# Performance work log

Hardware: AMD Instinct MI355X
Metric: run time of the kernel (lower is better)

The kernel has to match this reference:

```python
import jax, jax.numpy as jnp
import numpy as np

EMB = 1024
HEADS = 16
FFN = 4096
EPS = 1e-5


def _layernorm(x, g, b):
    mu = jnp.mean(x, axis=-1, keepdims=True)
    var = jnp.mean((x - mu) ** 2, axis=-1, keepdims=True)
    return (x - mu) * jax.lax.rsqrt(var + EPS) * g + b


def setup_inputs() -> dict:
    key = jax.random.key(0)
    ks = jax.random.split(key, 8)
    B, T = 2, 2048
    s_in = 1.0 / np.sqrt(EMB)
    s_ffn = 1.0 / np.sqrt(FFN)
    return {
        "x": jax.random.normal(ks[0], (B, T, EMB), jnp.float32),
        "positions": jnp.arange(B * T, dtype=jnp.int64 if jax.config.jax_enable_x64 else jnp.int32).reshape(B, T),
        "ln1_g": jnp.ones((EMB,), jnp.float32),
        "ln1_b": jnp.zeros((EMB,), jnp.float32),
        "ln2_g": jnp.ones((EMB,), jnp.float32),
        "ln2_b": jnp.zeros((EMB,), jnp.float32),
        "Wq": jax.random.normal(ks[1], (EMB, EMB), jnp.float32) * s_in,
        "bq": jnp.zeros((EMB,), jnp.float32),
        "Wk": jax.random.normal(ks[2], (EMB, EMB), jnp.float32) * s_in,
        "bk": jnp.zeros((EMB,), jnp.float32),
        "Wv": jax.random.normal(ks[3], (EMB, EMB), jnp.float32) * s_in,
        "bv": jnp.zeros((EMB,), jnp.float32),
        "Wo": jax.random.normal(ks[4], (EMB, EMB), jnp.float32) * s_in,
        "bo": jnp.zeros((EMB,), jnp.float32),
        "W1": jax.random.normal(ks[5], (EMB, FFN), jnp.float32) * s_in,
        "b1": jnp.zeros((FFN,), jnp.float32),
        "W2": jax.random.normal(ks[6], (FFN, EMB), jnp.float32) * s_ffn,
        "b2": jnp.zeros((EMB,), jnp.float32),
    }


def reference(x, positions, ln1_g, ln1_b, ln2_g, ln2_b,
              Wq, bq, Wk, bk, Wv, bv, Wo, bo, W1, b1, W2, b2):
    B, T, C = x.shape
    H, D = HEADS, C // HEADS
    # x = ln1(x); then residual branches add onto the normalized x (as in source)
    x = _layernorm(x, ln1_g, ln1_b)
    # --- self attention (rope=None, mask=None, dropout inactive) ---
    q = (x @ Wq + bq).reshape(B, T, H, D).transpose(0, 2, 1, 3)  # [B,H,T,D]
    k = (x @ Wk + bk).reshape(B, T, H, D).transpose(0, 2, 1, 3)
    v = (x @ Wv + bv).reshape(B, T, H, D).transpose(0, 2, 1, 3)
    scale = 1.0 / jnp.sqrt(jnp.asarray(D, x.dtype))
    attn = jnp.einsum("bhtd,bhsd->bhts", q, k) * scale  # [B,H,T,T]
    attn = jax.nn.softmax(attn, axis=-1)
    attn_out = jnp.einsum("bhts,bhsd->bhtd", attn, v)
    attn_out = attn_out.transpose(0, 2, 1, 3).reshape(B, T, C)
    attn_out = attn_out @ Wo + bo
    x = x + attn_out
    # --- FFN with exact (erf) GELU, matching torch nn.GELU default ---
    h = _layernorm(x, ln2_g, ln2_b)
    h = jax.nn.gelu(h @ W1 + b1, approximate=False)
    h = h @ W2 + b2
    return x + h
```

## Files before the change

### kernel.cpp

```cpp
#include <hip/hip_runtime.h>
#include <cstdint>
#include <cstddef>

typedef __bf16 bf16;
typedef __bf16 bf16x8 __attribute__((ext_vector_type(8)));
typedef __bf16 bf16x4 __attribute__((ext_vector_type(4)));
typedef float f32x4 __attribute__((ext_vector_type(4)));

#define TOKENS 4096
#define TSEQ   2048
#define NHEADS 16
#define HDIM   64
#define CDIM   1024

typedef __attribute__((address_space(3))) unsigned int lds_uint;
typedef __attribute__((address_space(1))) const unsigned int g_uint;
__device__ __forceinline__ void glds16(const bf16* g, bf16* l) {
  __builtin_amdgcn_global_load_lds((g_uint*)g, (lds_uint*)l, 16, 0, 0);
}

#define NBUF 17
struct DetectArgs { const void* p[NBUF]; int n[NBUF]; };

__global__ __launch_bounds__(256) void detect_kernel(DetectArgs a, int* __restrict__ flags) {
  __shared__ int s_nz, s_bl;
  if (threadIdx.x == 0) { s_nz = 0; s_bl = 0; }
  __syncthreads();
  int i = blockIdx.x;
  const unsigned int* w = (const unsigned int*)a.p[i];
  int nwords = a.n[i] / 2; if (nwords > 2048) nwords = 2048;
  int nz = 0, bl = 0;
  for (int j = threadIdx.x; j < nwords; j += 256) {
    unsigned int v = w[j];
    if (v != 0u) {
      nz++;
      unsigned int e = (v >> 7) & 0xFFu;
      if (e >= 100u && e <= 140u) bl++;
    }
  }
  atomicAdd(&s_nz, nz);
  atomicAdd(&s_bl, bl);
  __syncthreads();
  if (threadIdx.x == 0) flags[i] = (2 * s_bl >= s_nz) ? 1 : 0;
}

struct VecCvt { const void* p[10]; bf16* d[10]; int n[10]; int fi[10]; };
__global__ __launch_bounds__(256) void convert_vecs(VecCvt a, const int* __restrict__ flags) {
  int i = blockIdx.x;
  bool isb = flags[a.fi[i]] != 0;
  const void* in = a.p[i]; bf16* out = a.d[i]; int n = a.n[i];
  for (int j = threadIdx.x; j < n; j += 256)
    out[j] = isb ? ((const bf16*)in)[j] : (bf16)(((const float*)in)[j]);
}

__global__ __launch_bounds__(256) void transpose_any(const void* __restrict__ in,
                                                     bf16* __restrict__ out,
                                                     int K, int N,
                                                     const int* __restrict__ flag) {
  __shared__ bf16 tile[64][65];
  int kb = blockIdx.y * 64, nb = blockIdx.x * 64;
  int tx = threadIdx.x, ty = threadIdx.y;
  bool isb = (*flag != 0);
  for (int i = ty; i < 64; i += 4) {
    size_t idx = (size_t)(kb + i) * N + nb + tx;
    tile[i][tx] = isb ? ((const bf16*)in)[idx] : (bf16)(((const float*)in)[idx]);
  }
  __syncthreads();
  for (int i = ty; i < 64; i += 4)
    out[(size_t)(nb + i) * K + kb + tx] = tile[tx][i];
}

__device__ __forceinline__ void ln_body(const float (&v)[4], float s, float s2,
                                        const bf16* g, const bf16* b, bf16* yr, int tid) {
#pragma unroll
  for (int off = 32; off; off >>= 1) {
    s  += __shfl_down(s, off);
    s2 += __shfl_down(s2, off);
  }
  __shared__ float red[8];
  int w = tid >> 6;
  if ((tid & 63) == 0) { red[w] = s; red[4 + w] = s2; }
  __syncthreads();
  if (tid == 0) {
    red[0] = red[0] + red[1] + red[2] + red[3];
    red[4] = red[4] + red[5] + red[6] + red[7];
  }
  __syncthreads();
  float mu  = red[0] * (1.0f / CDIM);
  float var = fmaxf(red[4] * (1.0f / CDIM) - mu * mu, 0.f);
  float rstd = rsqrtf(var + 1e-5f);
#pragma unroll
  for (int i = 0; i < 4; i++) {
    int c = tid * 4 + i;
    yr[c] = (bf16)((v[i] - mu) * rstd * (float)g[c] + (float)b[c]);
  }
}

__global__ __launch_bounds__(256) void ln_any(const void* __restrict__ x,
                                              const int* __restrict__ flag,
                                              const bf16* __restrict__ g,
                                              const bf16* __restrict__ b,
                                              bf16* __restrict__ y) {
  int row = blockIdx.x, tid = threadIdx.x;
  bool isb = (*flag != 0);
  float v[4]; float s = 0.f, s2 = 0.f;
#pragma unroll
  for (int i = 0; i < 4; i++) {
    size_t idx = (size_t)row * CDIM + tid * 4 + i;
    float f = isb ? (float)((const bf16*)x)[idx] : ((const float*)x)[idx];
    v[i] = f; s += f; s2 += f * f;
  }
  ln_body(v, s, s2, g, b, y + (size_t)row * CDIM, tid);
}

__global__ __launch_bounds__(256) void ln_f32(const float* __restrict__ x,
                                              const bf16* __restrict__ g,
                                              const bf16* __restrict__ b,
                                              bf16* __restrict__ y) {
  int row = blockIdx.x, tid = threadIdx.x;
  float v[4]; float s = 0.f, s2 = 0.f;
#pragma unroll
  for (int i = 0; i < 4; i++) {
    float f = x[(size_t)row * CDIM + tid * 4 + i];
    v[i] = f; s += f; s2 += f * f;
  }
  ln_body(v, s, s2, g, b, y + (size_t)row * CDIM, tid);
}

template <int BM, int BN>
__device__ __forceinline__ void gemm_core(const bf16* __restrict__ A,
                                          const bf16* __restrict__ Bt,
                                          int K, int m0, int n0,
                                          bf16* As, bf16* Bs,
                                          f32x4 (&acc)[BM / 32][BN / 32]) {
  constexpr int SI = BM / 32, SJ = BN / 32;
  int t = threadIdx.x;
  int wave = t >> 6, lane = t & 63, quad = lane >> 4, l16 = lane & 15;
  int wm = (wave & 1) * (BM / 2), wn = (wave >> 1) * (BN / 2);
  int srow = t >> 2, sc = t & 3;
  int swz = (srow >> 1) & 3;
  const bf16* ga[BM / 64];
  const bf16* gb[BN / 64];
#pragma unroll
  for (int h = 0; h < BM / 64; h++)
    ga[h] = A + (size_t)(m0 + h * 64 + srow) * K + (sc ^ swz) * 8;
#pragma unroll
  for (int h = 0; h < BN / 64; h++)
    gb[h] = Bt + (size_t)(n0 + h * 64 + srow) * K + (sc ^ swz) * 8;

  for (int k0 = 0; k0 < K; k0 += 64) {
#pragma unroll
    for (int q = 0; q < 2; q++) {
#pragma unroll
      for (int h = 0; h < BM / 64; h++)
        glds16(ga[h] + k0 + q * 32, As + q * (BM * 32) + h * 2048 + srow * 32 + sc * 8);
#pragma unroll
      for (int h = 0; h < BN / 64; h++)
        glds16(gb[h] + k0 + q * 32, Bs + q * (BN * 32) + h * 2048 + srow * 32 + sc * 8);
    }
    __syncthreads();
#pragma unroll
    for (int q = 0; q < 2; q++) {
      bf16x8 af[SI], bfr[SJ];
#pragma unroll
      for (int i = 0; i < SI; i++) {
        int m = wm + i * 16 + l16;
        af[i] = *(const bf16x8*)&As[q * (BM * 32) + m * 32 + ((quad ^ ((m >> 1) & 3)) * 8)];
      }
#pragma unroll
      for (int j = 0; j < SJ; j++) {
        int n = wn + j * 16 + l16;
        bfr[j] = *(const bf16x8*)&Bs[q * (BN * 32) + n * 32 + ((quad ^ ((n >> 1) & 3)) * 8)];
      }
#pragma unroll
      for (int i = 0; i < SI; i++)
#pragma unroll
        for (int j = 0; j < SJ; j++)
          acc[i][j] = __builtin_amdgcn_mfma_f32_16x16x32_bf16(af[i], bfr[j], acc[i][j], 0, 0, 0);
    }
    __syncthreads();
  }
}

#define EPI_NONE 0
#define EPI_RES  1
#define EPI_GELU 2

template <int BM, int BN, int EPI, typename OutT, typename ResT>
__global__ __launch_bounds__(256) void gemm128(const bf16* __restrict__ A,
                                               const bf16* __restrict__ Bt,
                                               const bf16* __restrict__ bias,
                                               const ResT* __restrict__ res,
                                               OutT* __restrict__ C,
                                               int N, int K) {
  __shared__ alignas(16) bf16 As[2 * BM * 32];
  __shared__ alignas(16) bf16 Bs[2 * BN * 32];
  int m0 = blockIdx.y * BM, n0 = blockIdx.x * BN;
  f32x4 acc[BM / 32][BN / 32] = {};
  gemm_core<BM, BN>(A, Bt, K, m0, n0, As, Bs, acc);

  int t = threadIdx.x, wave = t >> 6, lane = t & 63, quad = lane >> 4, l16 = lane & 15;
  int wm = (wave & 1) * (BM / 2), wn = (wave >> 1) * (BN / 2);
#pragma unroll
  for (int i = 0; i < BM / 32; i++)
#pragma unroll
    for (int j = 0; j < BN / 32; j++) {
      int n = n0 + wn + j * 16 + l16;
      float bv = (float)bias[n];
#pragma unroll
      for (int r = 0; r < 4; r++) {
        int m = m0 + wm + i * 16 + quad * 4 + r;
        float v = acc[i][j][r] + bv;
        if (EPI == EPI_GELU)      v = 0.5f * v * (1.0f + erff(v * 0.70710678118654752f));
        else if (EPI == EPI_RES)  v += (float)res[(size_t)m * N + n];
        C[(size_t)m * N + n] = (OutT)v;
      }
    }
}

__global__ __launch_bounds__(256) void gemm_qkv(const bf16* __restrict__ A,
                                                const bf16* __restrict__ Bt,
                                                const bf16* __restrict__ bias,
                                                bf16* __restrict__ QK,
                                                bf16* __restrict__ Vt) {
  __shared__ alignas(16) bf16 As[2 * 128 * 32];
  __shared__ alignas(16) bf16 Bs[2 * 128 * 32];
  int m0 = blockIdx.y * 128, n0 = blockIdx.x * 128;
  f32x4 acc[4][4] = {};
  gemm_core<128, 128>(A, Bt, 1024, m0, n0, As, Bs, acc);

  int t = threadIdx.x, wave = t >> 6, lane = t & 63, quad = lane >> 4, l16 = lane & 15;
  int wm = (wave & 1) * 64, wn = (wave >> 1) * 64;
#pragma unroll
  for (int i = 0; i < 4; i++)
#pragma unroll
    for (int j = 0; j < 4; j++) {
      int n = n0 + wn + j * 16 + l16;
      float bv = (float)bias[n];
      int mb = m0 + wm + i * 16 + quad * 4;
      if (n < 1024) {
#pragma unroll
        for (int r = 0; r < 4; r++)
          QK[(size_t)(mb + r) * 2048 + n] = (bf16)((acc[i][j][r] + bv) * 0.125f);
      } else if (n < 2048) {
#pragma unroll
        for (int r = 0; r < 4; r++)
          QK[(size_t)(mb + r) * 2048 + n] = (bf16)(acc[i][j][r] + bv);
      } else {
        bf16x4 pk;
#pragma unroll
        for (int r = 0; r < 4; r++) pk[r] = (bf16)(acc[i][j][r] + bv);
        *(bf16x4*)&Vt[(size_t)(n - 2048) * TOKENS + mb] = pk;
      }
    }
}

__global__ __launch_bounds__(512) void attn_kernel(const bf16* __restrict__ QK,
                                                   const bf16* __restrict__ Vt,
                                                   bf16* __restrict__ O) {
  __shared__ alignas(16) bf16 Ks[2][4096];
  __shared__ alignas(16) bf16 Vs[2][4096];
  __shared__ alignas(16) bf16 Ps[8][16 * 72];
  int b = blockIdx.z, h = blockIdx.y, q0 = blockIdx.x * 128;
  int t = threadIdx.x, wave = t >> 6, lane = t & 63, quad = lane >> 4, l16 = lane & 15;

  const bf16* Qg = QK;
  const bf16* Kg = QK + 1024;
  const size_t bT = (size_t)b * TSEQ;
  const int h64 = h * 64;

  int srow = wave * 8 + (lane >> 3);
  int schunk = (lane & 7) ^ (srow & 7);

  bf16x8 aq0, aq1;
  {
    size_t qrow = bT + q0 + wave * 16 + l16;
    aq0 = *(const bf16x8*)&Qg[qrow * 2048 + h64 + quad * 8];
    aq1 = *(const bf16x8*)&Qg[qrow * 2048 + h64 + 32 + quad * 8];
  }

  f32x4 accO[4] = {};
  f32x4 accL = {};

  auto stage = [&](int tile, int buf) {
    glds16(&Kg[(bT + tile * 64 + srow) * 2048 + h64 + schunk * 8],
           &Ks[buf][wave * 512 + lane * 8]);
    glds16(&Vt[(size_t)(h64 + srow) * TOKENS + bT + tile * 64 + schunk * 8],
           &Vs[buf][wave * 512 + lane * 8]);
  };

  const bf16 one = (bf16)1.0f;
  const bf16x8 onesv = {one, one, one, one, one, one, one, one};
  int sw = l16 & 7;
  bf16* Pw = &Ps[wave][0];

  stage(0, 0);
  __syncthreads();

  for (int it = 0; it < TSEQ / 64; it++) {
    int cur = it & 1;
    if (it + 1 < TSEQ / 64) stage(it + 1, cur ^ 1);

    const bf16* KsC = &Ks[cur][0];
    const bf16* VsC = &Vs[cur][0];

    f32x4 S[4];
#pragma unroll
    for (int c = 0; c < 4; c++) {
      int row = c * 16 + l16;
      bf16x8 kb0 = *(const bf16x8*)&KsC[row * 64 + ((quad ^ sw) * 8)];
      bf16x8 kb1 = *(const bf16x8*)&KsC[row * 64 + (((quad + 4) ^ sw) * 8)];
      f32x4 s = {};
      s = __builtin_amdgcn_mfma_f32_16x16x32_bf16(aq0, kb0, s, 0, 0, 0);
      s = __builtin_amdgcn_mfma_f32_16x16x32_bf16(aq1, kb1, s, 0, 0, 0);
      S[c] = s;
    }

#pragma unroll
    for (int c = 0; c < 4; c++)
#pragma unroll
      for (int r = 0; r < 4; r++)
        Pw[(quad * 4 + r) * 72 + c * 16 + l16] = (bf16)__expf(fminf(S[c][r], 60.f));

    bf16x8 pa0 = *(const bf16x8*)&Pw[l16 * 72 + quad * 8];
    bf16x8 pa1 = *(const bf16x8*)&Pw[l16 * 72 + 32 + quad * 8];
#pragma unroll
    for (int ds = 0; ds < 4; ds++) {
      int row = ds * 16 + l16;
      bf16x8 vb0 = *(const bf16x8*)&VsC[row * 64 + ((quad ^ sw) * 8)];
      bf16x8 vb1 = *(const bf16x8*)&VsC[row * 64 + (((quad + 4) ^ sw) * 8)];
      accO[ds] = __builtin_amdgcn_mfma_f32_16x16x32_bf16(pa0, vb0, accO[ds], 0, 0, 0);
      accO[ds] = __builtin_amdgcn_mfma_f32_16x16x32_bf16(pa1, vb1, accO[ds], 0, 0, 0);
    }
    accL = __builtin_amdgcn_mfma_f32_16x16x32_bf16(pa0, onesv, accL, 0, 0, 0);
    accL = __builtin_amdgcn_mfma_f32_16x16x32_bf16(pa1, onesv, accL, 0, 0, 0);

    __syncthreads();
  }

#pragma unroll
  for (int ds = 0; ds < 4; ds++)
#pragma unroll
    for (int r = 0; r < 4; r++) {
      float v = accO[ds][r] / fmaxf(accL[r], 1e-30f);
      O[(bT + q0 + wave * 16 + quad * 4 + r) * CDIM + h64 + ds * 16 + l16] = (bf16)v;
    }
}

extern "C" void kernel_launch(void* const* d_in, const int* in_sizes, int n_in,
                              void* d_out, int out_size, void* d_ws, size_t ws_size,
                              hipStream_t stream) {
  char* ws = (char*)d_ws;
  const size_t MB = 1024 * 1024;
  const size_t KB = 1024;

  int* flags = (int*)ws;
  bf16* vec_c = (bf16*)(ws + 4 * KB);
  bf16* ln1g_c = vec_c + 0 * 8192;
  bf16* ln1b_c = vec_c + 1 * 8192;
  bf16* ln2g_c = vec_c + 2 * 8192;
  bf16* ln2b_c = vec_c + 3 * 8192;
  bf16* bqkv_c = vec_c + 4 * 8192;
  bf16* bo_c   = vec_c + 6 * 8192;
  bf16* b1_c   = vec_c + 7 * 8192;
  bf16* b2_c   = vec_c + 8 * 8192;

  bf16*  WqkvT  = (bf16*)(ws + 1 * MB);
  bf16*  WoT    = (bf16*)(ws + 7 * MB);
  bf16*  W1T    = (bf16*)(ws + 9 * MB);
  bf16*  W2T    = (bf16*)(ws + 17 * MB);
  bf16*  xn     = (bf16*)(ws + 25 * MB);
  bf16*  QKbuf  = (bf16*)(ws + 33 * MB);
  bf16*  Vtbuf  = (bf16*)(ws + 49 * MB);
  bf16*  ab     = (bf16*)(ws + 57 * MB);
  float* xmid32 = (float*)(ws + 65 * MB);
  bf16*  h2     = (bf16*)(ws + 81 * MB);
  bf16*  f1     = (bf16*)(ws + 33 * MB);

  const int din_idx[NBUF] = {0, 2, 3, 4, 5, 6, 7, 8, 9, 10, 11, 12, 13, 14, 15, 16, 17};
  DetectArgs da;
  for (int i = 0; i < NBUF; i++) { da.p[i] = d_in[din_idx[i]]; da.n[i] = in_sizes[din_idx[i]]; }
  detect_kernel<<<NBUF, 256, 0, stream>>>(da, flags);

  VecCvt vc;
  {
    const int vf[10] = {1, 2, 3, 4, 6, 8, 10, 12, 14, 16};
    bf16* vd[10] = {ln1g_c, ln1b_c, ln2g_c, ln2b_c,
                    bqkv_c, bqkv_c + 1024, bqkv_c + 2048, bo_c, b1_c, b2_c};
    for (int i = 0; i < 10; i++) {
      int di = din_idx[vf[i]];
      vc.p[i] = d_in[di]; vc.d[i] = vd[i]; vc.n[i] = in_sizes[di]; vc.fi[i] = vf[i];
    }
  }
  convert_vecs<<<10, 256, 0, stream>>>(vc, flags);

  dim3 tb(64, 4);
  transpose_any<<<dim3(16, 16), tb, 0, stream>>>(d_in[6],  WqkvT,                   1024, 1024, flags + 5);
  transpose_any<<<dim3(16, 16), tb, 0, stream>>>(d_in[8],  WqkvT + 1024 * 1024,     1024, 1024, flags + 7);
  transpose_any<<<dim3(16, 16), tb, 0, stream>>>(d_in[10], WqkvT + 2 * 1024 * 1024, 1024, 1024, flags + 9);
  transpose_any<<<dim3(16, 16), tb, 0, stream>>>(d_in[12], WoT, 1024, 1024, flags + 11);
  transpose_any<<<dim3(64, 16), tb, 0, stream>>>(d_in[14], W1T, 1024, 4096, flags + 13);
  transpose_any<<<dim3(16, 64), tb, 0, stream>>>(d_in[16], W2T, 4096, 1024, flags + 15);

  ln_any<<<TOKENS, 256, 0, stream>>>(d_in[0], flags + 0, ln1g_c, ln1b_c, xn);

  gemm_qkv<<<dim3(24, 32), 256, 0, stream>>>(xn, WqkvT, bqkv_c, QKbuf, Vtbuf);

  attn_kernel<<<dim3(TSEQ / 128, NHEADS, 2), 512, 0, stream>>>(QKbuf, Vtbuf, ab);

  gemm128<64, 128, EPI_RES, float, bf16><<<dim3(8, 64), 256, 0, stream>>>(
      ab, WoT, bo_c, xn, xmid32, 1024, 1024);

  ln_f32<<<TOKENS, 256, 0, stream>>>(xmid32, ln2g_c, ln2b_c, h2);

  gemm128<128, 128, EPI_GELU, bf16, bf16><<<dim3(32, 32), 256, 0, stream>>>(
      h2, W1T, b1_c, (const bf16*)nullptr, f1, 4096, 1024);

  gemm128<64, 128, EPI_RES, float, float><<<dim3(8, 64), 256, 0, stream>>>(
      f1, W2T, b2_c, xmid32, (float*)d_out, 1024, 4096);
}
```

Baseline: 453.7 us.

## Merge weight transposes, vector converts and first layernorm into one launch; use sigmoid GELU

Folds the six weight-transpose launches, the bias/gain conversion launch and the first layernorm into a single kernel whose block index picks the sub-task. This cuts launch overhead and lets the independent pieces run at the same time. The layernorm now reads gamma and beta straight from the raw inputs, so it no longer depends on the convert step. The exact erf GELU is replaced by a tanh-style approximation written with a sigmoid and __expf, which is cheaper per element but slightly changes numerics against the exact-GELU reference.

```diff
diff --git a/kernel.cpp b/kernel.cpp
--- a/kernel.cpp
+++ b/kernel.cpp
@@ -17,6 +17,11 @@
 typedef __attribute__((address_space(1))) const unsigned int g_uint;
 __device__ __forceinline__ void glds16(const bf16* g, bf16* l) {
   __builtin_amdgcn_global_load_lds((g_uint*)g, (lds_uint*)l, 16, 0, 0);
+}
+
+__device__ __forceinline__ float gelu_f(float v) {
+  float g2 = v * (1.5957691216f + 0.0713548163f * v * v);
+  return v / (1.0f + __expf(-g2));
 }
 
 #define NBUF 17
@@ -44,34 +49,11 @@
   if (threadIdx.x == 0) flags[i] = (2 * s_bl >= s_nz) ? 1 : 0;
 }
 
-struct VecCvt { const void* p[10]; bf16* d[10]; int n[10]; int fi[10]; };
-__global__ __launch_bounds__(256) void convert_vecs(VecCvt a, const int* __restrict__ flags) {
-  int i = blockIdx.x;
-  bool isb = flags[a.fi[i]] != 0;
-  const void* in = a.p[i]; bf16* out = a.d[i]; int n = a.n[i];
-  for (int j = threadIdx.x; j < n; j += 256)
-    out[j] = isb ? ((const bf16*)in)[j] : (bf16)(((const float*)in)[j]);
-}
-
-__global__ __launch_bounds__(256) void transpose_any(const void* __restrict__ in,
-                                                     bf16* __restrict__ out,
-                                                     int K, int N,
-                                                     const int* __restrict__ flag) {
-  __shared__ bf16 tile[64][65];
-  int kb = blockIdx.y * 64, nb = blockIdx.x * 64;
-  int tx = threadIdx.x, ty = threadIdx.y;
-  bool isb = (*flag != 0);
-  for (int i = ty; i < 64; i += 4) {
-    size_t idx = (size_t)(kb + i) * N + nb + tx;
-    tile[i][tx] = isb ? ((const bf16*)in)[idx] : (bf16)(((const float*)in)[idx]);
-  }
-  __syncthreads();
-  for (int i = ty; i < 64; i += 4)
-    out[(size_t)(nb + i) * K + kb + tx] = tile[tx][i];
-}
-
-__device__ __forceinline__ void ln_body(const float (&v)[4], float s, float s2,
-                                        const bf16* g, const bf16* b, bf16* yr, int tid) {
+__device__ __forceinline__ float ld_any(const void* p, size_t idx, bool isb) {
+  return isb ? (float)((const bf16*)p)[idx] : ((const float*)p)[idx];
+}
+
+__device__ __forceinline__ void ln_stats(float s, float s2, int tid, float& mu, float& rstd) {
 #pragma unroll
   for (int off = 32; off; off >>= 1) {
     s  += __shfl_down(s, off);
@@ -86,31 +68,9 @@
     red[4] = red[4] + red[5] + red[6] + red[7];
   }
   __syncthreads();
-  float mu  = red[0] * (1.0f / CDIM);
+  mu = red[0] * (1.0f / CDIM);
   float var = fmaxf(red[4] * (1.0f / CDIM) - mu * mu, 0.f);
-  float rstd = rsqrtf(var + 1e-5f);
-#pragma unroll
-  for (int i = 0; i < 4; i++) {
-    int c = tid * 4 + i;
-    yr[c] = (bf16)((v[i] - mu) * rstd * (float)g[c] + (float)b[c]);
-  }
-}
-
-__global__ __launch_bounds__(256) void ln_any(const void* __restrict__ x,
-                                              const int* __restrict__ flag,
-                                              const bf16* __restrict__ g,
-                                              const bf16* __restrict__ b,
-                                              bf16* __restrict__ y) {
-  int row = blockIdx.x, tid = threadIdx.x;
-  bool isb = (*flag != 0);
-  float v[4]; float s = 0.f, s2 = 0.f;
-#pragma unroll
-  for (int i = 0; i < 4; i++) {
-    size_t idx = (size_t)row * CDIM + tid * 4 + i;
-    float f = isb ? (float)((const bf16*)x)[idx] : ((const float*)x)[idx];
-    v[i] = f; s += f; s2 += f * f;
-  }
-  ln_body(v, s, s2, g, b, y + (size_t)row * CDIM, tid);
+  rstd = rsqrtf(var + 1e-5f);
 }
 
 __global__ __launch_bounds__(256) void ln_f32(const float* __restrict__ x,
@@ -124,7 +84,72 @@
     float f = x[(size_t)row * CDIM + tid * 4 + i];
     v[i] = f; s += f; s2 += f * f;
   }
-  ln_body(v, s, s2, g, b, y + (size_t)row * CDIM, tid);
+  float mu, rstd;
+  ln_stats(s, s2, tid, mu, rstd);
+  bf16* yr = y + (size_t)row * CDIM;
+#pragma unroll
+  for (int i = 0; i < 4; i++) {
+    int c = tid * 4 + i;
+    yr[c] = (bf16)((v[i] - mu) * rstd * (float)g[c] + (float)b[c]);
+  }
+}
+
+struct MegaArgs {
+  const void* w_in[6]; bf16* w_out[6]; int wK[6], wN[6], wflag[6];
+  const void* vp[10]; bf16* vd[10]; int vn[10], vfi[10];
+  const void* x; const void* graw; const void* braw; bf16* y;
+};
+
+__global__ __launch_bounds__(256) void mega_pre(MegaArgs a, const int* __restrict__ flags) {
+  int bid = blockIdx.x;
+  int tx = threadIdx.x, ty = threadIdx.y;
+  int tid = tx + ty * 64;
+  if (bid < 3072) {
+    __shared__ bf16 tile[64][65];
+    int mi, start;
+    if (bid < 1024)      { mi = bid >> 8; start = mi << 8; }
+    else if (bid < 2048) { mi = 4; start = 1024; }
+    else                 { mi = 5; start = 2048; }
+    int tb = bid - start;
+    int nT = a.wN[mi] >> 6;
+    int kb = (tb / nT) * 64, nb = (tb % nT) * 64;
+    int K = a.wK[mi], N = a.wN[mi];
+    bool isb = flags[a.wflag[mi]] != 0;
+    const void* in = a.w_in[mi]; bf16* out = a.w_out[mi];
+    for (int i = ty; i < 64; i += 4)
+      tile[i][tx] = (bf16)ld_any(in, (size_t)(kb + i) * N + nb + tx, isb);
+    __syncthreads();
+    for (int i = ty; i < 64; i += 4)
+      out[(size_t)(nb + i) * K + kb + tx] = tile[tx][i];
+  } else if (bid == 3072) {
+    for (int i = 0; i < 10; i++) {
+      bool isb = flags[a.vfi[i]] != 0;
+      const void* in = a.vp[i]; bf16* out = a.vd[i]; int n = a.vn[i];
+      for (int j = tid; j < n; j += 256)
+        out[j] = (bf16)ld_any(in, j, isb);
+    }
+  } else {
+    int row = bid - 3073;
+    bool isb  = flags[0] != 0;
+    bool gisb = flags[1] != 0;
+    bool bisb = flags[2] != 0;
+    float v[4]; float s = 0.f, s2 = 0.f;
+#pragma unroll
+    for (int i = 0; i < 4; i++) {
+      float f = ld_any(a.x, (size_t)row * CDIM + tid * 4 + i, isb);
+      v[i] = f; s += f; s2 += f * f;
+    }
+    float mu, rstd;
+    ln_stats(s, s2, tid, mu, rstd);
+    bf16* yr = a.y + (size_t)row * CDIM;
+#pragma unroll
+    for (int i = 0; i < 4; i++) {
+      int c = tid * 4 + i;
+      float gv = ld_any(a.graw, c, gisb);
+      float bv = ld_any(a.braw, c, bisb);
+      yr[c] = (bf16)((v[i] - mu) * rstd * gv + bv);
+    }
+  }
 }
 
 template <int BM, int BN>
@@ -211,7 +236,7 @@
       for (int r = 0; r < 4; r++) {
         int m = m0 + wm + i * 16 + quad * 4 + r;
         float v = acc[i][j][r] + bv;
-        if (EPI == EPI_GELU)      v = 0.5f * v * (1.0f + erff(v * 0.70710678118654752f));
+        if (EPI == EPI_GELU)      v = gelu_f(v);
         else if (EPI == EPI_RES)  v += (float)res[(size_t)m * N + n];
         C[(size_t)m * N + n] = (OutT)v;
       }
@@ -382,27 +407,27 @@
   for (int i = 0; i < NBUF; i++) { da.p[i] = d_in[din_idx[i]]; da.n[i] = in_sizes[din_idx[i]]; }
   detect_kernel<<<NBUF, 256, 0, stream>>>(da, flags);
 
-  VecCvt vc;
+  MegaArgs ma;
   {
+    const void* wi[6] = {d_in[6], d_in[8], d_in[10], d_in[12], d_in[14], d_in[16]};
+    bf16* wo[6] = {WqkvT, WqkvT + 1024 * 1024, WqkvT + 2 * 1024 * 1024, WoT, W1T, W2T};
+    const int wK[6] = {1024, 1024, 1024, 1024, 1024, 4096};
+    const int wN[6] = {1024, 1024, 1024, 1024, 4096, 1024};
+    const int wf[6] = {5, 7, 9, 11, 13, 15};
+    for (int i = 0; i < 6; i++) {
+      ma.w_in[i] = wi[i]; ma.w_out[i] = wo[i];
+      ma.wK[i] = wK[i]; ma.wN[i] = wN[i]; ma.wflag[i] = wf[i];
+    }
     const int vf[10] = {1, 2, 3, 4, 6, 8, 10, 12, 14, 16};
     bf16* vd[10] = {ln1g_c, ln1b_c, ln2g_c, ln2b_c,
                     bqkv_c, bqkv_c + 1024, bqkv_c + 2048, bo_c, b1_c, b2_c};
     for (int i = 0; i < 10; i++) {
       int di = din_idx[vf[i]];
-      vc.p[i] = d_in[di]; vc.d[i] = vd[i]; vc.n[i] = in_sizes[di]; vc.fi[i] = vf[i];
-    }
-  }
-  convert_vecs<<<10, 256, 0, stream>>>(vc, flags);
-
-  dim3 tb(64, 4);
-  transpose_any<<<dim3(16, 16), tb, 0, stream>>>(d_in[6],  WqkvT,                   1024, 1024, flags + 5);
-  transpose_any<<<dim3(16, 16), tb, 0, stream>>>(d_in[8],  WqkvT + 1024 * 1024,     1024, 1024, flags + 7);
-  transpose_any<<<dim3(16, 16), tb, 0, stream>>>(d_in[10], WqkvT + 2 * 1024 * 1024, 1024, 1024, flags + 9);
-  transpose_any<<<dim3(16, 16), tb, 0, stream>>>(d_in[12], WoT, 1024, 1024, flags + 11);
-  transpose_any<<<dim3(64, 16), tb, 0, stream>>>(d_in[14], W1T, 1024, 4096, flags + 13);
-  transpose_any<<<dim3(16, 64), tb, 0, stream>>>(d_in[16], W2T, 4096, 1024, flags + 15);
-
-  ln_any<<<TOKENS, 256, 0, stream>>>(d_in[0], flags + 0, ln1g_c, ln1b_c, xn);
+      ma.vp[i] = d_in[di]; ma.vd[i] = vd[i]; ma.vn[i] = in_sizes[di]; ma.vfi[i] = vf[i];
+    }
+    ma.x = d_in[0]; ma.graw = d_in[2]; ma.braw = d_in[3]; ma.y = xn;
+  }
+  mega_pre<<<3072 + 1 + TOKENS, dim3(64, 4), 0, stream>>>(ma, flags);
 
   gemm_qkv<<<dim3(24, 32), 256, 0, stream>>>(xn, WqkvT, bqkv_c, QKbuf, Vtbuf);
 
```

Result: faster. 395.8 us (-12.8%).
